# Kernel optimization log

Measured on AMD Instinct MI355X. Metric: run time of the kernel, lower is better.

## Reference

```python
import jax, jax.numpy as jnp
import numpy as np

NEG_INF = jnp.finfo(jnp.float32).min


def setup_inputs() -> dict:
    key = jax.random.key(0)
    ks = jax.random.split(key, 5)
    B, S, D = 2, 2048, 1024
    std = 0.02
    return {
        "x": jax.random.normal(ks[0], (B, S, D), dtype=jnp.float32),
        "attention_mask": jnp.ones((B, S), dtype=jnp.int32),
        "Wq": jax.random.normal(ks[1], (D, D), dtype=jnp.float32) * std,
        "Wk": jax.random.normal(ks[2], (D, D), dtype=jnp.float32) * std,
        "Wv": jax.random.normal(ks[3], (D, D), dtype=jnp.float32) * std,
        "Wo": jax.random.normal(ks[4], (D, D), dtype=jnp.float32) * std,
    }


def reference(x, attention_mask, Wq, Wk, Wv, Wo):
    B, S, D = x.shape
    H = 16
    Hd = D // H
    scale = jnp.float32(np.sqrt(Hd))

    # F.linear uses W @ x^T, i.e. x @ W.T
    def proj(x, W):
        return jnp.einsum('bsd,ed->bse', x, W).reshape(B, S, H, Hd).transpose(0, 2, 1, 3)

    q = proj(x, Wq)  # [B,H,S,Hd]
    k = proj(x, Wk)
    v = proj(x, Wv)

    scores = jnp.einsum('bhqd,bhkd->bhqk', q, k) / scale  # [B,H,S,S]
    causal = jnp.triu(jnp.ones((S, S), dtype=bool), k=1)
    scores = jnp.where(causal[None, None, :, :], NEG_INF, scores)
    key_pad = (attention_mask == 0)[:, None, None, :]  # [B,1,1,S]
    scores = jnp.where(key_pad, NEG_INF, scores)

    attn = jax.nn.softmax(scores, axis=-1)
    out = jnp.einsum('bhqk,bhkd->bhqd', attn, v)  # [B,H,S,Hd]
    out = out.transpose(0, 2, 1, 3).reshape(B, S, D)
    return jnp.einsum('bsd,ed->bse', out, Wo)
```

## Files before the change

### kernel.cpp

```cpp
#include <hip/hip_runtime.h>
#include <hip/hip_bf16.h>

typedef __attribute__((ext_vector_type(8))) short bf16x8;
typedef __attribute__((ext_vector_type(4))) short bf16x4;
typedef __attribute__((ext_vector_type(4))) float f32x4;

#define LOG2E 1.4426950408889634f
#define NEGF  -3.0e38f

__device__ __forceinline__ void gl_lds16(const void* g, void* l) {
  __builtin_amdgcn_global_load_lds((const __attribute__((address_space(1))) void*)g,
                                   (__attribute__((address_space(3))) void*)l, 16, 0, 0);
}

__device__ __forceinline__ ushort f2bu(float x) {
  __hip_bfloat16 h = __float2bfloat16(x);
  return *(ushort*)&h;
}

__global__ __launch_bounds__(256) void cast_bf16_k(const float* __restrict__ in,
                                                   ushort* __restrict__ out, int n4) {
  int i = blockIdx.x * 256 + threadIdx.x;
  if (i >= n4) return;
  float4 f = ((const float4*)in)[i];
  ushort4 u;
  u.x = f2bu(f.x); u.y = f2bu(f.y); u.z = f2bu(f.z); u.w = f2bu(f.w);
  ((ushort4*)out)[i] = u;
}

__global__ __launch_bounds__(256) void cast_w4_k(const float* __restrict__ a, const float* __restrict__ b,
                                                 const float* __restrict__ c, const float* __restrict__ d,
                                                 ushort* __restrict__ oa, ushort* __restrict__ ob,
                                                 ushort* __restrict__ oc, ushort* __restrict__ od) {
  int i = blockIdx.x * 256 + threadIdx.x;
  int wsel = i >> 18, j = i & 262143;
  const float* src = wsel == 0 ? a : wsel == 1 ? b : wsel == 2 ? c : d;
  ushort* dst      = wsel == 0 ? oa : wsel == 1 ? ob : wsel == 2 ? oc : od;
  float4 f = ((const float4*)src)[j];
  ushort4 u;
  u.x = f2bu(f.x); u.y = f2bu(f.y); u.z = f2bu(f.z); u.w = f2bu(f.w);
  ((ushort4*)dst)[j] = u;
}

template<int OUT_BF16>
__device__ __forceinline__ void gemm_body(const ushort* __restrict__ A, const ushort* __restrict__ B,
                                          void* __restrict__ C, int M, int N, int Kd, float scale,
                                          int bm, int bn, ushort (*As)[4096], ushort (*Bs)[4096]) {
  const int t  = threadIdx.x;
  const int l  = t & 63;
  const int w  = t >> 6;
  const int lr = l & 15, lg = l >> 4;
  const int wr = (w >> 1) * 64, wc = (w & 1) * 64;

  auto stage = [&](int buf, int ktE) {
    int idx = t, row = idx >> 2, ch = idx & 3;
    gl_lds16(A + (size_t)(bm + row) * Kd + ktE + ch * 8, &As[buf][idx * 8]);
    gl_lds16(B + (size_t)(bn + row) * Kd + ktE + ch * 8, &Bs[buf][idx * 8]);
    idx = t + 256; row = idx >> 2; ch = idx & 3;
    gl_lds16(A + (size_t)(bm + row) * Kd + ktE + ch * 8, &As[buf][idx * 8]);
    gl_lds16(B + (size_t)(bn + row) * Kd + ktE + ch * 8, &Bs[buf][idx * 8]);
  };

  f32x4 acc[4][4] = {};
  const int nK = Kd >> 5;

  stage(0, 0);
  stage(1, 32);
  int cur = 0;
  for (int k5 = 0; k5 < nK; ++k5) {
    if (k5 + 2 < nK) {
      int nb = cur + 2; if (nb >= 3) nb -= 3;
      stage(nb, (k5 + 2) << 5);
      asm volatile("s_waitcnt vmcnt(8)" ::: "memory");
    } else if (k5 + 1 < nK) {
      asm volatile("s_waitcnt vmcnt(4)" ::: "memory");
    } else {
      asm volatile("s_waitcnt vmcnt(0)" ::: "memory");
    }
    __builtin_amdgcn_s_barrier();

    bf16x8 af[4], bfr[4];
#pragma unroll
    for (int m = 0; m < 4; ++m)
      af[m] = *(const bf16x8*)&As[cur][(wr + m * 16 + lr) * 32 + lg * 8];
#pragma unroll
    for (int n = 0; n < 4; ++n)
      bfr[n] = *(const bf16x8*)&Bs[cur][(wc + n * 16 + lr) * 32 + lg * 8];
#pragma unroll
    for (int m = 0; m < 4; ++m)
#pragma unroll
      for (int n = 0; n < 4; ++n)
        acc[m][n] = __builtin_amdgcn_mfma_f32_16x16x32_bf16(af[m], bfr[n], acc[m][n], 0, 0, 0);

    __builtin_amdgcn_s_barrier();
    ++cur; if (cur >= 3) cur -= 3;
  }

#pragma unroll
  for (int m = 0; m < 4; ++m)
#pragma unroll
    for (int n = 0; n < 4; ++n)
#pragma unroll
      for (int j = 0; j < 4; ++j) {
        int row = bm + wr + m * 16 + lg * 4 + j;
        int col = bn + wc + n * 16 + lr;
        float v = acc[m][n][j] * scale;
        if (OUT_BF16) {
          ((ushort*)C)[(size_t)row * N + col] = f2bu(v);
        } else {
          ((float*)C)[(size_t)row * N + col] = v;
        }
      }
}

__global__ __launch_bounds__(256)
void gemm_bt_f32(const ushort* __restrict__ A, const ushort* __restrict__ B, float* __restrict__ C,
                 int M, int N, int Kd, float scale) {
  __shared__ __attribute__((aligned(16))) ushort As[3][4096];
  __shared__ __attribute__((aligned(16))) ushort Bs[3][4096];
  gemm_body<0>(A, B, C, M, N, Kd, scale, blockIdx.x * 128, blockIdx.y * 128, As, Bs);
}

__global__ __launch_bounds__(256)
void gemm_qkv(const ushort* __restrict__ A, const ushort* __restrict__ Wq, const ushort* __restrict__ Wk,
              const ushort* __restrict__ Wv, ushort* __restrict__ Qo, ushort* __restrict__ Ko,
              ushort* __restrict__ Vo, int M, int Kd) {
  __shared__ __attribute__((aligned(16))) ushort As[3][4096];
  __shared__ __attribute__((aligned(16))) ushort Bs[3][4096];
  int by = blockIdx.y;
  int which = by >> 3;
  const ushort* B = which == 0 ? Wq : which == 1 ? Wk : Wv;
  ushort* C       = which == 0 ? Qo : which == 1 ? Ko : Vo;
  float scale = which == 0 ? 0.125f : 1.0f;
  gemm_body<1>(A, B, C, M, 1024, Kd, scale, blockIdx.x * 128, (by & 7) * 128, As, Bs);
}

__device__ __forceinline__ void online_sm(f32x4 s4[4], float& m_, float& l_, f32x4 o[4],
                                          int lg, bf16x8& pa0_out, bf16x8& pa1_out) {
  float tm = NEGF;
#pragma unroll
  for (int c = 0; c < 4; ++c)
#pragma unroll
    for (int j = 0; j < 4; ++j) tm = fmaxf(tm, s4[c][j]);
  tm = fmaxf(tm, __shfl_xor(tm, 16));
  tm = fmaxf(tm, __shfl_xor(tm, 32));

  bool need = !__all(tm - m_ <= 8.0f);
  float mn = need ? fmaxf(m_, tm) : m_;
  float scl = mn * LOG2E;
  if (need) {
    float alpha = exp2f(m_ * LOG2E - scl);
    m_ = mn;
    l_ *= alpha;
    float a0 = __shfl(alpha, lg * 4 + 0, 16);
    float a1 = __shfl(alpha, lg * 4 + 1, 16);
    float a2 = __shfl(alpha, lg * 4 + 2, 16);
    float a3 = __shfl(alpha, lg * 4 + 3, 16);
#pragma unroll
    for (int dt = 0; dt < 4; ++dt) {
      o[dt][0] *= a0; o[dt][1] *= a1; o[dt][2] *= a2; o[dt][3] *= a3;
    }
  }

  float rs = 0.f;
#pragma unroll
  for (int c = 0; c < 4; ++c)
#pragma unroll
    for (int j = 0; j < 4; ++j) {
      float p = exp2f(s4[c][j] * LOG2E - scl);
      rs += p;
      s4[c][j] = p;
    }
  rs += __shfl_xor(rs, 16);
  rs += __shfl_xor(rs, 32);
  l_ += rs;

  union { bf16x8 v; ushort u[8]; } pa0, pa1;
#pragma unroll
  for (int j = 0; j < 4; ++j) {
    pa0.u[j]     = f2bu(s4[0][j]);
    pa0.u[4 + j] = f2bu(s4[1][j]);
    pa1.u[j]     = f2bu(s4[2][j]);
    pa1.u[4 + j] = f2bu(s4[3][j]);
  }
  pa0_out = pa0.v;
  pa1_out = pa1.v;
}

__global__ __launch_bounds__(512, 4)
void attn_k(const ushort* __restrict__ Q, const ushort* __restrict__ K,
            const ushort* __restrict__ V, const int* __restrict__ mask,
            ushort* __restrict__ O) {
  const int S = 2048, D = 1024;
  __shared__ __attribute__((aligned(16))) ushort Ks[4][4096];
  __shared__ __attribute__((aligned(16))) ushort Vs[4][4096];
  __shared__ unsigned long long Msb[32];

  const int t = threadIdx.x;
  const int l = t & 63, w = t >> 6;
  const int wi = w & 3;
  const int wg = w >> 2;
  const int lr = l & 15, lg = l >> 4;

  int f = blockIdx.x;
  int pp = (f >> 3) & 15;
  int p  = ((f >> 8) & 1) ? 15 - pp : pp;
  int bh = (f & 7) | ((f >> 7) << 3);
  int h = bh & 15, b = bh >> 4;
  const int qA = p, qB = 31 - p;
  const int nt = qB + 1;
  const int qt = wg ? qB : qA;
  const size_t bS = (size_t)b * S;

  const ushort* qptr = Q + (bS + qt * 64 + wi * 16 + lr) * D + h * 64;
  bf16x8 qf0 = *(const bf16x8*)(qptr + lg * 8);
  bf16x8 qf1 = *(const bf16x8*)(qptr + 32 + lg * 8);

  const ushort* Kbh = K + bS * D + h * 64;
  const ushort* Vbh = V + bS * D + h * 64;
  const int* mbase = mask + bS;

  for (int kk = w; kk < nt; kk += 8) {
    unsigned long long mb = __ballot(mbase[kk * 64 + l] != 0);
    if (l == 0) Msb[kk] = mb;
  }
  asm volatile("s_waitcnt lgkmcnt(0)" ::: "memory");
  __builtin_amdgcn_sched_barrier(0);

  float m_ = -INFINITY, l_ = 0.f;
  f32x4 o[4] = {};

  auto stage = [&](int buf, int kt) {
    { int idx = t; int row = idx >> 3, ch = idx & 7;
      gl_lds16(Kbh + (size_t)(kt * 64 + row) * D + ((ch ^ (row & 7)) * 8), &Ks[buf][idx * 8]); }
    { int idx = t; int dg = idx >> 7, kq = (idx >> 3) & 15, jj = (idx >> 1) & 3, hf = idx & 1;
      gl_lds16(Vbh + (size_t)(kt * 64 + kq * 4 + jj) * D + dg * 16 + hf * 8, &Vs[buf][idx * 8]); }
  };

  stage(0, 0);
  stage(1, 1);

  for (int kt = 0; kt < nt; ++kt) {
    const int cur = kt & 3;
    if (kt + 2 < nt) {
      stage((kt + 2) & 3, kt + 2);
      asm volatile("s_waitcnt vmcnt(4)" ::: "memory");
    } else if (kt + 1 < nt) {
      asm volatile("s_waitcnt vmcnt(2)" ::: "memory");
    } else {
      asm volatile("s_waitcnt vmcnt(0)" ::: "memory");
    }
    __builtin_amdgcn_s_barrier();

    if (kt <= qt) {
      unsigned long long mb = Msb[kt];
      const bool diag = (kt == qt);
      const int cmax = diag ? wi : 3;

      f32x4 s4[4];
      __builtin_amdgcn_s_setprio(1);
#pragma unroll
      for (int c = 0; c < 4; ++c) {
        if (c <= cmax) {
          int row = c * 16 + lr;
          bf16x8 kf0 = *(const bf16x8*)&Ks[cur][row * 64 + ((lg ^ (row & 7)) << 3)];
          bf16x8 kf1 = *(const bf16x8*)&Ks[cur][row * 64 + (((4 + lg) ^ (row & 7)) << 3)];
          f32x4 sc = {0.f, 0.f, 0.f, 0.f};
          sc = __builtin_amdgcn_mfma_f32_16x16x32_bf16(kf0, qf0, sc, 0, 0, 0);
          sc = __builtin_amdgcn_mfma_f32_16x16x32_bf16(kf1, qf1, sc, 0, 0, 0);
          if (diag && c == cmax) {
            int qg = wi * 16 + lr, kb = c * 16 + lg * 4;
#pragma unroll
            for (int j = 0; j < 4; ++j)
              if (kb + j > qg) sc[j] = NEGF;
          }
          s4[c] = sc;
        } else {
          s4[c] = (f32x4){NEGF, NEGF, NEGF, NEGF};
        }
      }
      __builtin_amdgcn_s_setprio(0);

      if (~mb != 0ull) {
#pragma unroll
        for (int c = 0; c < 4; ++c)
#pragma unroll
          for (int j = 0; j < 4; ++j)
            if (!((mb >> (c * 16 + lg * 4 + j)) & 1)) s4[c][j] = NEGF;
      }

      bf16x8 pa0, pa1;
      online_sm(s4, m_, l_, o, lg, pa0, pa1);

      __builtin_amdgcn_s_setprio(1);
#pragma unroll
      for (int dt = 0; dt < 4; ++dt) {
        const __attribute__((address_space(3))) ushort* vp =
            (const __attribute__((address_space(3))) ushort*)&Vs[cur][0] + dt * 1024 + lg * 64 + lr * 4;
        bf16x4 h0, h1, h2, h3;
        asm volatile(
            "ds_read_b64_tr_b16 %0, %4\n\t"
            "ds_read_b64_tr_b16 %1, %4 offset:512\n\t"
            "ds_read_b64_tr_b16 %2, %4 offset:1024\n\t"
            "ds_read_b64_tr_b16 %3, %4 offset:1536\n\t"
            "s_waitcnt lgkmcnt(0)"
            : "=&v"(h0), "=&v"(h1), "=&v"(h2), "=&v"(h3)
            : "v"(vp));
        bf16x8 vb0 = __builtin_shufflevector(h0, h1, 0, 1, 2, 3, 4, 5, 6, 7);
        bf16x8 vb1 = __builtin_shufflevector(h2, h3, 0, 1, 2, 3, 4, 5, 6, 7);
        o[dt] = __builtin_amdgcn_mfma_f32_16x16x32_bf16(pa0, vb0, o[dt], 0, 0, 0);
        o[dt] = __builtin_amdgcn_mfma_f32_16x16x32_bf16(pa1, vb1, o[dt], 0, 0, 0);
      }
      __builtin_amdgcn_s_setprio(0);
    }
  }

  float inv = 1.0f / l_;
  float v0 = __shfl(inv, lg * 4 + 0, 16);
  float v1 = __shfl(inv, lg * 4 + 1, 16);
  float v2 = __shfl(inv, lg * 4 + 2, 16);
  float v3 = __shfl(inv, lg * 4 + 3, 16);
#pragma unroll
  for (int dt = 0; dt < 4; ++dt) {
    size_t col = (size_t)h * 64 + dt * 16 + lr;
    size_t r0 = bS + qt * 64 + wi * 16 + lg * 4;
    O[(r0 + 0) * D + col] = f2bu(o[dt][0] * v0);
    O[(r0 + 1) * D + col] = f2bu(o[dt][1] * v1);
    O[(r0 + 2) * D + col] = f2bu(o[dt][2] * v2);
    O[(r0 + 3) * D + col] = f2bu(o[dt][3] * v3);
  }
}

extern "C" void kernel_launch(void* const* d_in, const int* in_sizes, int n_in,
                              void* d_out, int out_size, void* d_ws, size_t ws_size,
                              hipStream_t stream) {
  const float* x    = (const float*)d_in[0];
  const int*   mask = (const int*)d_in[1];
  const float* Wq   = (const float*)d_in[2];
  const float* Wk   = (const float*)d_in[3];
  const float* Wv   = (const float*)d_in[4];
  const float* Wo   = (const float*)d_in[5];
  float* out = (float*)d_out;

  const int B = 2, S = 2048, D = 1024;
  const int M = B * S;

  char* ws = (char*)d_ws;
  ushort* xb  = (ushort*)(ws);
  ushort* wqb = (ushort*)(ws + (8ull  << 20));
  ushort* wkb = (ushort*)(ws + (10ull << 20));
  ushort* wvb = (ushort*)(ws + (12ull << 20));
  ushort* wob = (ushort*)(ws + (14ull << 20));
  ushort* Qb  = (ushort*)(ws + (16ull << 20));
  ushort* Kb  = (ushort*)(ws + (24ull << 20));
  ushort* Vb  = (ushort*)(ws + (32ull << 20));
  ushort* AO  = (ushort*)(ws + (40ull << 20));

  int nx4 = M * D / 4;
  cast_bf16_k<<<(nx4 + 255) / 256, 256, 0, stream>>>(x, xb, nx4);
  cast_w4_k<<<4096, 256, 0, stream>>>(Wq, Wk, Wv, Wo, wqb, wkb, wvb, wob);

  dim3 gq(M / 128, 24);
  gemm_qkv<<<gq, 256, 0, stream>>>(xb, wqb, wkb, wvb, Qb, Kb, Vb, M, D);

  attn_k<<<512, 512, 0, stream>>>(Qb, Kb, Vb, mask, AO);

  dim3 gp(M / 128, D / 128);
  gemm_bt_f32<<<gp, 256, 0, stream>>>(AO, wob, out, M, D, D, 1.0f);
}
```

Measured before the change: 122.9 us.

## Process two adjacent query tiles per wave to reuse K/V fragments

```diff
diff --git a/kernel.cpp b/kernel.cpp
--- a/kernel.cpp
+++ b/kernel.cpp
@@ -187,147 +187,176 @@
   pa1_out = pa1.v;
 }
 
-__global__ __launch_bounds__(512, 4)
+__global__ __launch_bounds__(256, 3)
 void attn_k(const ushort* __restrict__ Q, const ushort* __restrict__ K,
             const ushort* __restrict__ V, const int* __restrict__ mask,
             ushort* __restrict__ O) {
   const int S = 2048, D = 1024;
-  __shared__ __attribute__((aligned(16))) ushort Ks[4][4096];
-  __shared__ __attribute__((aligned(16))) ushort Vs[4][4096];
+  __shared__ __attribute__((aligned(16))) ushort Ks[3][4096];
+  __shared__ __attribute__((aligned(16))) ushort Vs[3][4096];
   __shared__ unsigned long long Msb[32];
 
   const int t = threadIdx.x;
-  const int l = t & 63, w = t >> 6;
-  const int wi = w & 3;
-  const int wg = w >> 2;
+  const int l = t & 63, wi = t >> 6;
   const int lr = l & 15, lg = l >> 4;
 
   int f = blockIdx.x;
-  int pp = (f >> 3) & 15;
-  int p  = ((f >> 8) & 1) ? 15 - pp : pp;
-  int bh = (f & 7) | ((f >> 7) << 3);
+  int s3 = (f >> 3) & 7;
+  int ss = ((f >> 8) & 1) ? 15 - s3 : s3;
+  int bh = (f & 7) | (((f >> 6) & 3) << 3);
   int h = bh & 15, b = bh >> 4;
-  const int qA = p, qB = 31 - p;
-  const int nt = qB + 1;
-  const int qt = wg ? qB : qA;
+  const int nt = 2 * ss + 2;
   const size_t bS = (size_t)b * S;
-
-  const ushort* qptr = Q + (bS + qt * 64 + wi * 16 + lr) * D + h * 64;
-  bf16x8 qf0 = *(const bf16x8*)(qptr + lg * 8);
-  bf16x8 qf1 = *(const bf16x8*)(qptr + 32 + lg * 8);
+  const int q0 = ss * 128;
+
+  const ushort* qpL = Q + (bS + q0 + wi * 16 + lr) * D + h * 64;
+  const ushort* qpU = qpL + (size_t)64 * D;
+  bf16x8 qL0 = *(const bf16x8*)(qpL + lg * 8);
+  bf16x8 qL1 = *(const bf16x8*)(qpL + 32 + lg * 8);
+  bf16x8 qU0 = *(const bf16x8*)(qpU + lg * 8);
+  bf16x8 qU1 = *(const bf16x8*)(qpU + 32 + lg * 8);
 
   const ushort* Kbh = K + bS * D + h * 64;
   const ushort* Vbh = V + bS * D + h * 64;
   const int* mbase = mask + bS;
 
-  for (int kk = w; kk < nt; kk += 8) {
+  for (int kk = wi; kk < nt; kk += 4) {
     unsigned long long mb = __ballot(mbase[kk * 64 + l] != 0);
     if (l == 0) Msb[kk] = mb;
   }
   asm volatile("s_waitcnt lgkmcnt(0)" ::: "memory");
   __builtin_amdgcn_sched_barrier(0);
 
-  float m_ = -INFINITY, l_ = 0.f;
-  f32x4 o[4] = {};
+  float mL = -INFINITY, lL = 0.f, mU = -INFINITY, lU = 0.f;
+  f32x4 oL[4] = {}, oU[4] = {};
 
   auto stage = [&](int buf, int kt) {
-    { int idx = t; int row = idx >> 3, ch = idx & 7;
+    { int idx = t;       int row = idx >> 3, ch = idx & 7;
+      gl_lds16(Kbh + (size_t)(kt * 64 + row) * D + ((ch ^ (row & 7)) * 8), &Ks[buf][idx * 8]);
+      idx = t + 256; row = idx >> 3; ch = idx & 7;
       gl_lds16(Kbh + (size_t)(kt * 64 + row) * D + ((ch ^ (row & 7)) * 8), &Ks[buf][idx * 8]); }
-    { int idx = t; int dg = idx >> 7, kq = (idx >> 3) & 15, jj = (idx >> 1) & 3, hf = idx & 1;
+    { int idx = t;  int dg = idx >> 7, kq = (idx >> 3) & 15, jj = (idx >> 1) & 3, hf = idx & 1;
+      gl_lds16(Vbh + (size_t)(kt * 64 + kq * 4 + jj) * D + dg * 16 + hf * 8, &Vs[buf][idx * 8]);
+      idx = t + 256; dg = idx >> 7; kq = (idx >> 3) & 15; jj = (idx >> 1) & 3; hf = idx & 1;
       gl_lds16(Vbh + (size_t)(kt * 64 + kq * 4 + jj) * D + dg * 16 + hf * 8, &Vs[buf][idx * 8]); }
   };
 
   stage(0, 0);
-  stage(1, 1);
-
+  if (nt > 1) stage(1, 1);
+
+  int cur = 0;
   for (int kt = 0; kt < nt; ++kt) {
-    const int cur = kt & 3;
-    if (kt + 2 < nt) {
-      stage((kt + 2) & 3, kt + 2);
-      asm volatile("s_waitcnt vmcnt(4)" ::: "memory");
-    } else if (kt + 1 < nt) {
-      asm volatile("s_waitcnt vmcnt(2)" ::: "memory");
-    } else {
-      asm volatile("s_waitcnt vmcnt(0)" ::: "memory");
-    }
+    if (kt + 1 < nt) asm volatile("s_waitcnt vmcnt(4)" ::: "memory");
+    else             asm volatile("s_waitcnt vmcnt(0)" ::: "memory");
     __builtin_amdgcn_s_barrier();
-
-    if (kt <= qt) {
-      unsigned long long mb = Msb[kt];
-      const bool diag = (kt == qt);
-      const int cmax = diag ? wi : 3;
-
-      f32x4 s4[4];
-      __builtin_amdgcn_s_setprio(1);
-#pragma unroll
-      for (int c = 0; c < 4; ++c) {
-        if (c <= cmax) {
-          int row = c * 16 + lr;
-          bf16x8 kf0 = *(const bf16x8*)&Ks[cur][row * 64 + ((lg ^ (row & 7)) << 3)];
-          bf16x8 kf1 = *(const bf16x8*)&Ks[cur][row * 64 + (((4 + lg) ^ (row & 7)) << 3)];
+    if (kt + 2 < nt) stage((cur + 2 >= 3) ? cur - 1 : cur + 2, kt + 2);
+
+    const bool diagU = (kt == nt - 1);
+    const bool actL  = (kt <  nt - 1);
+    const bool diagL = (kt == nt - 2);
+    unsigned long long mb = Msb[kt];
+
+    f32x4 sU[4], sL[4];
+    __builtin_amdgcn_s_setprio(1);
+#pragma unroll
+    for (int c = 0; c < 4; ++c) {
+      int row = c * 16 + lr;
+      bf16x8 kf0 = *(const bf16x8*)&Ks[cur][row * 64 + ((lg ^ (row & 7)) << 3)];
+      bf16x8 kf1 = *(const bf16x8*)&Ks[cur][row * 64 + (((4 + lg) ^ (row & 7)) << 3)];
+      if (!diagU || c <= wi) {
+        f32x4 sc = {0.f, 0.f, 0.f, 0.f};
+        sc = __builtin_amdgcn_mfma_f32_16x16x32_bf16(kf0, qU0, sc, 0, 0, 0);
+        sc = __builtin_amdgcn_mfma_f32_16x16x32_bf16(kf1, qU1, sc, 0, 0, 0);
+        if (diagU && c == wi) {
+          int qg = wi * 16 + lr, kb = c * 16 + lg * 4;
+#pragma unroll
+          for (int j = 0; j < 4; ++j)
+            if (kb + j > qg) sc[j] = NEGF;
+        }
+        sU[c] = sc;
+      } else {
+        sU[c] = (f32x4){NEGF, NEGF, NEGF, NEGF};
+      }
+      if (actL) {
+        if (!diagL || c <= wi) {
           f32x4 sc = {0.f, 0.f, 0.f, 0.f};
-          sc = __builtin_amdgcn_mfma_f32_16x16x32_bf16(kf0, qf0, sc, 0, 0, 0);
-          sc = __builtin_amdgcn_mfma_f32_16x16x32_bf16(kf1, qf1, sc, 0, 0, 0);
-          if (diag && c == cmax) {
+          sc = __builtin_amdgcn_mfma_f32_16x16x32_bf16(kf0, qL0, sc, 0, 0, 0);
+          sc = __builtin_amdgcn_mfma_f32_16x16x32_bf16(kf1, qL1, sc, 0, 0, 0);
+          if (diagL && c == wi) {
             int qg = wi * 16 + lr, kb = c * 16 + lg * 4;
 #pragma unroll
             for (int j = 0; j < 4; ++j)
               if (kb + j > qg) sc[j] = NEGF;
           }
-          s4[c] = sc;
+          sL[c] = sc;
         } else {
-          s4[c] = (f32x4){NEGF, NEGF, NEGF, NEGF};
+          sL[c] = (f32x4){NEGF, NEGF, NEGF, NEGF};
         }
       }
-      __builtin_amdgcn_s_setprio(0);
-
-      if (~mb != 0ull) {
-#pragma unroll
-        for (int c = 0; c < 4; ++c)
-#pragma unroll
-          for (int j = 0; j < 4; ++j)
-            if (!((mb >> (c * 16 + lg * 4 + j)) & 1)) s4[c][j] = NEGF;
+    }
+    __builtin_amdgcn_s_setprio(0);
+
+    if (~mb != 0ull) {
+#pragma unroll
+      for (int c = 0; c < 4; ++c)
+#pragma unroll
+        for (int j = 0; j < 4; ++j) {
+          bool z = !((mb >> (c * 16 + lg * 4 + j)) & 1);
+          if (z) sU[c][j] = NEGF;
+          if (actL && z) sL[c][j] = NEGF;
+        }
+    }
+
+    bf16x8 paU0, paU1, paL0, paL1;
+    online_sm(sU, mU, lU, oU, lg, paU0, paU1);
+    if (actL) online_sm(sL, mL, lL, oL, lg, paL0, paL1);
+
+    __builtin_amdgcn_s_setprio(1);
+#pragma unroll
+    for (int dt = 0; dt < 4; ++dt) {
+      const __attribute__((address_space(3))) ushort* vp =
+          (const __attribute__((address_space(3))) ushort*)&Vs[cur][0] + dt * 1024 + lg * 64 + lr * 4;
+      bf16x4 h0, h1, h2, h3;
+      asm volatile(
+          "ds_read_b64_tr_b16 %0, %4\n\t"
+          "ds_read_b64_tr_b16 %1, %4 offset:512\n\t"
+          "ds_read_b64_tr_b16 %2, %4 offset:1024\n\t"
+          "ds_read_b64_tr_b16 %3, %4 offset:1536\n\t"
+          "s_waitcnt lgkmcnt(0)"
+          : "=&v"(h0), "=&v"(h1), "=&v"(h2), "=&v"(h3)
+          : "v"(vp));
+      bf16x8 vb0 = __builtin_shufflevector(h0, h1, 0, 1, 2, 3, 4, 5, 6, 7);
+      bf16x8 vb1 = __builtin_shufflevector(h2, h3, 0, 1, 2, 3, 4, 5, 6, 7);
+      oU[dt] = __builtin_amdgcn_mfma_f32_16x16x32_bf16(paU0, vb0, oU[dt], 0, 0, 0);
+      oU[dt] = __builtin_amdgcn_mfma_f32_16x16x32_bf16(paU1, vb1, oU[dt], 0, 0, 0);
+      if (actL) {
+        oL[dt] = __builtin_amdgcn_mfma_f32_16x16x32_bf16(paL0, vb0, oL[dt], 0, 0, 0);
+        oL[dt] = __builtin_amdgcn_mfma_f32_16x16x32_bf16(paL1, vb1, oL[dt], 0, 0, 0);
       }
-
-      bf16x8 pa0, pa1;
-      online_sm(s4, m_, l_, o, lg, pa0, pa1);
-
-      __builtin_amdgcn_s_setprio(1);
-#pragma unroll
-      for (int dt = 0; dt < 4; ++dt) {
-        const __attribute__((address_space(3))) ushort* vp =
-            (const __attribute__((address_space(3))) ushort*)&Vs[cur][0] + dt * 1024 + lg * 64 + lr * 4;
-        bf16x4 h0, h1, h2, h3;
-        asm volatile(
-            "ds_read_b64_tr_b16 %0, %4\n\t"
-            "ds_read_b64_tr_b16 %1, %4 offset:512\n\t"
-            "ds_read_b64_tr_b16 %2, %4 offset:1024\n\t"
-            "ds_read_b64_tr_b16 %3, %4 offset:1536\n\t"
-            "s_waitcnt lgkmcnt(0)"
-            : "=&v"(h0), "=&v"(h1), "=&v"(h2), "=&v"(h3)
-            : "v"(vp));
-        bf16x8 vb0 = __builtin_shufflevector(h0, h1, 0, 1, 2, 3, 4, 5, 6, 7);
-        bf16x8 vb1 = __builtin_shufflevector(h2, h3, 0, 1, 2, 3, 4, 5, 6, 7);
-        o[dt] = __builtin_amdgcn_mfma_f32_16x16x32_bf16(pa0, vb0, o[dt], 0, 0, 0);
-        o[dt] = __builtin_amdgcn_mfma_f32_16x16x32_bf16(pa1, vb1, o[dt], 0, 0, 0);
-      }
-      __builtin_amdgcn_s_setprio(0);
-    }
-  }
-
-  float inv = 1.0f / l_;
-  float v0 = __shfl(inv, lg * 4 + 0, 16);
-  float v1 = __shfl(inv, lg * 4 + 1, 16);
-  float v2 = __shfl(inv, lg * 4 + 2, 16);
-  float v3 = __shfl(inv, lg * 4 + 3, 16);
-#pragma unroll
-  for (int dt = 0; dt < 4; ++dt) {
-    size_t col = (size_t)h * 64 + dt * 16 + lr;
-    size_t r0 = bS + qt * 64 + wi * 16 + lg * 4;
-    O[(r0 + 0) * D + col] = f2bu(o[dt][0] * v0);
-    O[(r0 + 1) * D + col] = f2bu(o[dt][1] * v1);
-    O[(r0 + 2) * D + col] = f2bu(o[dt][2] * v2);
-    O[(r0 + 3) * D + col] = f2bu(o[dt][3] * v3);
+    }
+    __builtin_amdgcn_s_setprio(0);
+
+    ++cur; if (cur >= 3) cur -= 3;
+  }
+
+#pragma unroll
+  for (int grp = 0; grp < 2; ++grp) {
+    float l_ = grp ? lU : lL;
+    f32x4* o = grp ? oU : oL;
+    float inv = 1.0f / l_;
+    float v0 = __shfl(inv, lg * 4 + 0, 16);
+    float v1 = __shfl(inv, lg * 4 + 1, 16);
+    float v2 = __shfl(inv, lg * 4 + 2, 16);
+    float v3 = __shfl(inv, lg * 4 + 3, 16);
+    size_t rbase = bS + q0 + grp * 64 + wi * 16 + lg * 4;
+#pragma unroll
+    for (int dt = 0; dt < 4; ++dt) {
+      size_t col = (size_t)h * 64 + dt * 16 + lr;
+      O[(rbase + 0) * D + col] = f2bu(o[dt][0] * v0);
+      O[(rbase + 1) * D + col] = f2bu(o[dt][1] * v1);
+      O[(rbase + 2) * D + col] = f2bu(o[dt][2] * v2);
+      O[(rbase + 3) * D + col] = f2bu(o[dt][3] * v3);
+    }
   }
 }
 
@@ -363,7 +392,7 @@
   dim3 gq(M / 128, 24);
   gemm_qkv<<<gq, 256, 0, stream>>>(xb, wqb, wkb, wvb, Qb, Kb, Vb, M, D);
 
-  attn_k<<<512, 512, 0, stream>>>(Qb, Kb, Vb, mask, AO);
+  attn_k<<<512, 256, 0, stream>>>(Qb, Kb, Vb, mask, AO);
 
   dim3 gp(M / 128, D / 128);
   gemm_bt_f32<<<gp, 256, 0, stream>>>(AO, wob, out, M, D, D, 1.0f);
```

Measured after the change: 137.1 us. 1.11x slower.
